# Performance work log

Hardware: AMD Instinct MI355X
Metric: run time of the kernel (lower is better)

## Reference

```python
import jax, jax.numpy as jnp
import numpy as np

B, IN, H = 4096, 512, 1024
ALPHA, RHO = 0.001, 0.05

def setup_inputs() -> dict:
    key = jax.random.key(0)
    ks = jax.random.split(key, 9)
    inp = jax.random.normal(ks[0], (B, IN), dtype=jnp.float32)
    time = jax.random.uniform(ks[1], (B, 1), dtype=jnp.float32) * 100.0
    hx = jax.random.normal(ks[2], (B, H), dtype=jnp.float32)
    cx = jax.random.normal(ks[3], (B, H), dtype=jnp.float32)
    # params (match torch init scales loosely)
    Wxh_w = jax.random.normal(ks[4], (4 * H, IN), dtype=jnp.float32) / np.sqrt(IN)
    Wxh_b = jnp.zeros((4 * H,), dtype=jnp.float32)
    Whh_w = jax.random.normal(ks[5], (4 * H, H), dtype=jnp.float32) / np.sqrt(H)
    tau = jax.random.normal(ks[6], (H,), dtype=jnp.float32) * 0.5 + 5.0
    s = jax.random.uniform(ks[7], (H,), dtype=jnp.float32) * tau
    alpha = jnp.array([ALPHA], dtype=jnp.float32)
    rho = jnp.array([RHO], dtype=jnp.float32)
    return {"input": inp, "time": time, "hx": hx, "cx": cx,
            "Wxh_w": Wxh_w, "Wxh_b": Wxh_b, "Whh_w": Whh_w,
            "tau": tau, "s": s, "alpha": alpha, "rho": rho}

def _time_gate(time, s, tau, alpha, rho):
    # phi: [B, H] (time [B,1] broadcast against s/tau [H])
    phi = jnp.fmod(time - s, tau) / tau
    k = jnp.where(phi < rho / 2.0, 2.0 * phi / rho,
        jnp.where(phi < rho, 2.0 - 2.0 * phi / rho, alpha * phi))
    # computed under torch.no_grad() in the original
    return jax.lax.stop_gradient(k)

def reference(input, time, hx, cx, Wxh_w, Wxh_b, Whh_w, tau, s, alpha, rho):
    gates = input @ Wxh_w.T + Wxh_b + hx @ Whh_w.T  # [B, 4H]
    i, f, g, o = jnp.split(gates, 4, axis=1)
    k = _time_gate(time, s, tau, alpha, rho)
    ft = jax.nn.sigmoid(f + 1.0 - k)
    it = jax.nn.sigmoid(i) * k
    gt = jnp.tanh(g) * k
    ot = jax.nn.sigmoid(o) * k
    cy = ft * cx + it * gt
    hy = ot * jnp.tanh(cy)
    return (hy, cy)
```

## Files before the change

### kernel.cpp

```cpp
#include <hip/hip_runtime.h>

#define AS1 __attribute__((address_space(1)))
#define AS3 __attribute__((address_space(3)))

typedef _Float16 half_t;
typedef __attribute__((ext_vector_type(8))) _Float16 f16x8;
typedef __attribute__((ext_vector_type(4))) float f32x4;

static constexpr int Bsz = 4096;
static constexpr int INs = 512;
static constexpr int Hs  = 1024;
static constexpr int BM  = 128;
static constexpr int BH  = 32;
static constexpr int BK  = 64;

static constexpr size_t XN  = (size_t)Bsz * INs;
static constexpr size_t HXN = (size_t)Bsz * Hs;
static constexpr size_t WXN = (size_t)4 * Hs * INs;
static constexpr size_t WHN = (size_t)4 * Hs * Hs;
static constexpr size_t OFF_X  = 0;
static constexpr size_t OFF_HX = XN;
static constexpr size_t OFF_WX = XN + HXN;
static constexpr size_t OFF_WH = XN + HXN + WXN;
static constexpr size_t TOT    = XN + HXN + WXN + WHN;

__device__ __forceinline__ float sigm(float x) {
  return 1.0f / (1.0f + __expf(-x));
}
__device__ __forceinline__ float tanh_fast(float x) {
  const float e = __expf(2.0f * x);
  return 1.0f - 2.0f / (e + 1.0f);
}

__global__ __launch_bounds__(256)
void cvt_kernel(const float* __restrict__ x, const float* __restrict__ hx,
                const float* __restrict__ wx, const float* __restrict__ wh,
                half_t* __restrict__ ws) {
  const size_t cid = (size_t)blockIdx.x * 256 + threadIdx.x;
  const size_t e = cid * 8;
  const float* src; size_t off;
  if (e < OFF_HX)      { src = x;  off = e - OFF_X; }
  else if (e < OFF_WX) { src = hx; off = e - OFF_HX; }
  else if (e < OFF_WH) { src = wx; off = e - OFF_WX; }
  else                 { src = wh; off = e - OFF_WH; }
  const f32x4 a = *(const f32x4*)(src + off);
  const f32x4 b = *(const f32x4*)(src + off + 4);
  f16x8 o;
  o[0]=(half_t)a[0]; o[1]=(half_t)a[1]; o[2]=(half_t)a[2]; o[3]=(half_t)a[3];
  o[4]=(half_t)b[0]; o[5]=(half_t)b[1]; o[6]=(half_t)b[2]; o[7]=(half_t)b[3];
  *(f16x8*)(ws + e) = o;
}


#define KSTEP(Abase, vA, Wbase, vB, Ka_, t_) do { \
  _Pragma("unroll") \
  for (int i_ = 0; i_ < 4; ++i_) { \
    const int e_ = i_ * 32 + ldr; \
    const half_t* ga_ = (Abase) + (vA) + (i_ * 32 * (Ka_) + (t_) * BK); \
    __builtin_amdgcn_global_load_lds((AS1 void*)ga_, \
        (AS3 void*)(As + (e_ * 8 + ldc) * 8), 16, 0, 0); \
    const half_t* gw_ = (Wbase) + (vB)[i_] + ((t_) * BK); \
    __builtin_amdgcn_global_load_lds((AS1 void*)gw_, \
        (AS3 void*)(Bs + (e_ * 8 + ldc) * 8), 16, 0, 0); \
  } \
  __syncthreads(); \
  _Pragma("unroll") \
  for (int kk_ = 0; kk_ < 2; ++kk_) { \
    const int c8x_ = kk_ * 4 + grp; \
    f16x8 af_[4], bf_[4]; \
    _Pragma("unroll") \
    for (int mt_ = 0; mt_ < 4; ++mt_) { \
      const int e_ = wr * 64 + mt_ * 16 + l15; \
      af_[mt_] = *(const f16x8*)(As + (e_ * 8 + (c8x_ ^ (l15 & 7))) * 8); \
    } \
    _Pragma("unroll") \
    for (int nt_ = 0; nt_ < 4; ++nt_) { \
      const int e_ = wc * 64 + nt_ * 16 + l15; \
      bf_[nt_] = *(const f16x8*)(Bs + (e_ * 8 + (c8x_ ^ (l15 & 7))) * 8); \
    } \
    _Pragma("unroll") \
    for (int mt_ = 0; mt_ < 4; ++mt_) \
      _Pragma("unroll") \
      for (int nt_ = 0; nt_ < 4; ++nt_) \
        acc[mt_][nt_] = __builtin_amdgcn_mfma_f32_16x16x32_f16( \
            af_[mt_], bf_[nt_], acc[mt_][nt_], 0, 0, 0); \
  } \
  __syncthreads(); \
} while (0)

__global__ __launch_bounds__(256, 4)
void plstm_gemm(const half_t* __restrict__ xin,
                const half_t* __restrict__ hxp,
                const float* __restrict__ cxp,
                const half_t* __restrict__ wxh,
                const float* __restrict__ biasp,
                const half_t* __restrict__ whh,
                const float* __restrict__ timep,
                const float* __restrict__ taup,
                const float* __restrict__ sp,
                const float* __restrict__ alphap,
                const float* __restrict__ rhop,
                float* __restrict__ outp)
{
  __shared__ half_t As[BM * BK];
  __shared__ half_t Bs[BM * BK];

  const int tid  = threadIdx.x;
  const int w    = tid >> 6;
  const int lane = tid & 63;
  const int l15  = lane & 15;
  const int grp  = lane >> 4;
  const int wr   = w >> 1;
  const int wc   = w & 1;

  const int m0 = blockIdx.x * BM;
  const int h0 = blockIdx.y * BH;

  f32x4 acc[4][4] = {};

  const int ldr = tid >> 3;
  const int ldc = tid & 7;
  const int gc8 = ldc ^ (ldr & 7);

  {
    const half_t* Ab = xin + (size_t)m0 * INs;
    const int vA = ldr * INs + gc8 * 8;
    int vB[4];
    #pragma unroll
    for (int i = 0; i < 4; ++i) {
      const int gi = (2 * i + (ldr >> 4)) & 3;
      vB[i] = (gi * Hs + h0 + (i >> 1) * 16 + (ldr & 15)) * INs + gc8 * 8;
    }
    #pragma unroll
    for (int t = 0; t < INs / BK; ++t)
      KSTEP(Ab, vA, wxh, vB, INs, t);
  }
  {
    const half_t* Ab = hxp + (size_t)m0 * Hs;
    const int vA = ldr * Hs + gc8 * 8;
    int vB[4];
    #pragma unroll
    for (int i = 0; i < 4; ++i) {
      const int gi = (2 * i + (ldr >> 4)) & 3;
      vB[i] = (gi * Hs + h0 + (i >> 1) * 16 + (ldr & 15)) * Hs + gc8 * 8;
    }
    #pragma unroll
    for (int t = 0; t < Hs / BK; ++t)
      KSTEP(Ab, vA, whh, vB, Hs, t);
  }

  const int h = h0 + wc * 16 + l15;
  const float bi  = biasp[h];
  const float bfv = biasp[Hs + h];
  const float bg  = biasp[2 * Hs + h];
  const float bo  = biasp[3 * Hs + h];
  const float sv = sp[h], tauv = taup[h];
  const float alphav = alphap[0], rhov = rhop[0], rh = 0.5f * rhov;
  const float rtau   = 1.0f / tauv;
  const float tworho = 2.0f / rhov;

  #pragma unroll
  for (int mt = 0; mt < 4; ++mt) {
    const f32x4 t4 = *(const f32x4*)(timep + m0 + wr * 64 + mt * 16 + grp * 4);
    #pragma unroll
    for (int r = 0; r < 4; ++r) {
      const int brow = m0 + wr * 64 + mt * 16 + grp * 4 + r;
      const float q   = (t4[r] - sv) * rtau;
      const float phi = q - truncf(q);
      const float kv  = phi < rh   ? phi * tworho
                      : (phi < rhov ? 2.0f - phi * tworho
                                    : alphav * phi);

      const float iv = acc[mt][0][r] + bi;
      const float fv = acc[mt][1][r] + bfv;
      const float gv = acc[mt][2][r] + bg;
      const float ov = acc[mt][3][r] + bo;
      const float cxv = cxp[(size_t)brow * Hs + h];
      const float ft = sigm(fv + 1.0f - kv);
      const float it2 = sigm(iv) * kv;
      const float gt = tanh_fast(gv) * kv;
      const float ot = sigm(ov) * kv;
      const float cy = ft * cxv + it2 * gt;
      const float hy = ot * tanh_fast(cy);

      outp[(size_t)brow * Hs + h] = hy;
      outp[(size_t)Bsz * Hs + (size_t)brow * Hs + h] = cy;
    }
  }
}

__global__ __launch_bounds__(256, 3)
void plstm_gemm_f32(const float* __restrict__ xin, const float* __restrict__ timep,
                    const float* __restrict__ hxp, const float* __restrict__ cxp,
                    const float* __restrict__ wxh, const float* __restrict__ biasp,
                    const float* __restrict__ whh, const float* __restrict__ taup,
                    const float* __restrict__ sp, const float* __restrict__ alphap,
                    const float* __restrict__ rhop, float* __restrict__ outp)
{
  __shared__ half_t As[BM * BK];
  __shared__ half_t Bs[BM * BK];

  const int tid  = threadIdx.x;
  const int w    = tid >> 6;
  const int lane = tid & 63;
  const int l15  = lane & 15;
  const int grp  = lane >> 4;
  const int wr   = w >> 1;
  const int wc   = w & 1;

  const int m0 = blockIdx.x * BM;
  const int h0 = blockIdx.y * BH;

  f32x4 acc[4][4] = {};
  const int ldr = tid >> 3;
  const int ldc = tid & 7;
  const int NIT = INs / BK + Hs / BK;

  for (int it = 0; it < NIT; ++it) {
    const bool p1 = it >= INs / BK;
    const float* Ap = p1 ? hxp : xin;
    const float* Wp = p1 ? whh : wxh;
    const int Ka = p1 ? Hs : INs;
    const int k0 = (p1 ? (it - INs / BK) : it) * BK;
    #pragma unroll
    for (int i = 0; i < 4; ++i) {
      const int e    = i * 32 + ldr;
      const int gc8  = ldc ^ (e & 7);
      const int wrow = ((e >> 4) & 3) * Hs + h0 + ((e >> 6) << 4) + (e & 15);
      const float* ga = Ap + (size_t)(m0 + e) * Ka + (k0 + gc8 * 8);
      const f32x4 a0v = *(const f32x4*)ga, a1v = *(const f32x4*)(ga + 4);
      f16x8 pa;
      pa[0]=(half_t)a0v[0]; pa[1]=(half_t)a0v[1]; pa[2]=(half_t)a0v[2]; pa[3]=(half_t)a0v[3];
      pa[4]=(half_t)a1v[0]; pa[5]=(half_t)a1v[1]; pa[6]=(half_t)a1v[2]; pa[7]=(half_t)a1v[3];
      *(f16x8*)(As + (e * 8 + ldc) * 8) = pa;
      const float* gw = Wp + (size_t)wrow * Ka + (k0 + gc8 * 8);
      const f32x4 b0v = *(const f32x4*)gw, b1v = *(const f32x4*)(gw + 4);
      f16x8 pb;
      pb[0]=(half_t)b0v[0]; pb[1]=(half_t)b0v[1]; pb[2]=(half_t)b0v[2]; pb[3]=(half_t)b0v[3];
      pb[4]=(half_t)b1v[0]; pb[5]=(half_t)b1v[1]; pb[6]=(half_t)b1v[2]; pb[7]=(half_t)b1v[3];
      *(f16x8*)(Bs + (e * 8 + ldc) * 8) = pb;
    }
    __syncthreads();
    #pragma unroll
    for (int kk = 0; kk < 2; ++kk) {
      const int c8x = kk * 4 + grp;
      f16x8 af[4], bfr[4];
      #pragma unroll
      for (int mt = 0; mt < 4; ++mt) {
        const int e = wr * 64 + mt * 16 + l15;
        af[mt] = *(const f16x8*)(As + (e * 8 + (c8x ^ (l15 & 7))) * 8);
      }
      #pragma unroll
      for (int nt = 0; nt < 4; ++nt) {
        const int e = wc * 64 + nt * 16 + l15;
        bfr[nt] = *(const f16x8*)(Bs + (e * 8 + (c8x ^ (l15 & 7))) * 8);
      }
      #pragma unroll
      for (int mt = 0; mt < 4; ++mt)
        #pragma unroll
        for (int nt = 0; nt < 4; ++nt)
          acc[mt][nt] = __builtin_amdgcn_mfma_f32_16x16x32_f16(
              af[mt], bfr[nt], acc[mt][nt], 0, 0, 0);
    }
    __syncthreads();
  }

  const int h = h0 + wc * 16 + l15;
  const float bi  = biasp[h];
  const float bfv = biasp[Hs + h];
  const float bg  = biasp[2 * Hs + h];
  const float bo  = biasp[3 * Hs + h];
  const float sv = sp[h], tauv = taup[h];
  const float alphav = alphap[0], rhov = rhop[0], rh = 0.5f * rhov;
  const float rtau   = 1.0f / tauv;
  const float tworho = 2.0f / rhov;

  #pragma unroll
  for (int mt = 0; mt < 4; ++mt) {
    const f32x4 t4 = *(const f32x4*)(timep + m0 + wr * 64 + mt * 16 + grp * 4);
    #pragma unroll
    for (int r = 0; r < 4; ++r) {
      const int brow = m0 + wr * 64 + mt * 16 + grp * 4 + r;
      const float q   = (t4[r] - sv) * rtau;
      const float phi = q - truncf(q);
      const float kv  = phi < rh   ? phi * tworho
                      : (phi < rhov ? 2.0f - phi * tworho
                                    : alphav * phi);
      const float iv = acc[mt][0][r] + bi;
      const float fv = acc[mt][1][r] + bfv;
      const float gv = acc[mt][2][r] + bg;
      const float ov = acc[mt][3][r] + bo;
      const float cxv = cxp[(size_t)brow * Hs + h];
      const float ft = sigm(fv + 1.0f - kv);
      const float it2 = sigm(iv) * kv;
      const float gt = tanh_fast(gv) * kv;
      const float ot = sigm(ov) * kv;
      const float cy = ft * cxv + it2 * gt;
      const float hy = ot * tanh_fast(cy);
      outp[(size_t)brow * Hs + h] = hy;
      outp[(size_t)Bsz * Hs + (size_t)brow * Hs + h] = cy;
    }
  }
}

extern "C" void kernel_launch(void* const* d_in, const int* in_sizes, int n_in,
                              void* d_out, int out_size, void* d_ws, size_t ws_size,
                              hipStream_t stream) {
  (void)in_sizes; (void)n_in; (void)out_size;
  const float* xin   = (const float*)d_in[0];
  const float* timep = (const float*)d_in[1];
  const float* hxp   = (const float*)d_in[2];
  const float* cxp   = (const float*)d_in[3];
  const float* wxh   = (const float*)d_in[4];
  const float* biasp = (const float*)d_in[5];
  const float* whh   = (const float*)d_in[6];
  const float* taup  = (const float*)d_in[7];
  const float* sp    = (const float*)d_in[8];
  const float* alphap= (const float*)d_in[9];
  const float* rhop  = (const float*)d_in[10];
  float* outp = (float*)d_out;

  dim3 grid(Bsz / BM, Hs / BH);
  if (ws_size >= TOT * sizeof(half_t)) {
    half_t* ws = (half_t*)d_ws;
    cvt_kernel<<<(int)(TOT / 8 / 256), 256, 0, stream>>>(xin, hxp, wxh, whh, ws);
    plstm_gemm<<<grid, 256, 0, stream>>>(
        ws + OFF_X, ws + OFF_HX, cxp, ws + OFF_WX, biasp, ws + OFF_WH,
        timep, taup, sp, alphap, rhop, outp);
  } else {
    plstm_gemm_f32<<<grid, 256, 0, stream>>>(
        xin, timep, hxp, cxp, wxh, biasp, whh,
        taup, sp, alphap, rhop, outp);
  }
}
```

Before: 180.8 us.

## Double-buffer weight tiles in LDS and load activations directly to registers

The fp16 GEMM kernel stops staging the activation tile through LDS. Each wave now loads its A fragments straight from global memory into registers. Only the weight tile goes through LDS, now in two buffers, so the next k-step's weights are prefetched with global_load_lds while the current step's MFMAs run, leaving one barrier per step instead of two. Occupancy hint drops from 4 to 3 blocks per SM because the extra register fragments and the doubled B buffer raise register and LDS use; direct global A loads may also be less coalesced than the old LDS staging.

```diff
diff --git a/kernel.cpp b/kernel.cpp
--- a/kernel.cpp
+++ b/kernel.cpp
@@ -52,43 +52,40 @@
 }
 
 
-#define KSTEP(Abase, vA, Wbase, vB, Ka_, t_) do { \
+#define GSTEP(bufR, bufW, Ab, vA0, KaA, Wsrc, vBv, STAGE_EN) do { \
+  f16x8 af_[4][2]; \
   _Pragma("unroll") \
-  for (int i_ = 0; i_ < 4; ++i_) { \
-    const int e_ = i_ * 32 + ldr; \
-    const half_t* ga_ = (Abase) + (vA) + (i_ * 32 * (Ka_) + (t_) * BK); \
-    __builtin_amdgcn_global_load_lds((AS1 void*)ga_, \
-        (AS3 void*)(As + (e_ * 8 + ldc) * 8), 16, 0, 0); \
-    const half_t* gw_ = (Wbase) + (vB)[i_] + ((t_) * BK); \
-    __builtin_amdgcn_global_load_lds((AS1 void*)gw_, \
-        (AS3 void*)(Bs + (e_ * 8 + ldc) * 8), 16, 0, 0); \
-  } \
-  __syncthreads(); \
+  for (int mt_ = 0; mt_ < 4; ++mt_) \
+    _Pragma("unroll") \
+    for (int kk_ = 0; kk_ < 2; ++kk_) \
+      af_[mt_][kk_] = *(const f16x8*)((Ab) + (size_t)(mt_ * 16 * (KaA)) + (vA0) + kk_ * 32); \
+  if (STAGE_EN) { \
+    _Pragma("unroll") \
+    for (int i_ = 0; i_ < 4; ++i_) { \
+      const int e_ = i_ * 32 + ldr; \
+      __builtin_amdgcn_global_load_lds((AS1 void*)((Wsrc) + (vBv)[i_]), \
+          (AS3 void*)((bufW) + (e_ * 8 + ldc) * 8), 16, 0, 0); \
+    } } \
   _Pragma("unroll") \
   for (int kk_ = 0; kk_ < 2; ++kk_) { \
     const int c8x_ = kk_ * 4 + grp; \
-    f16x8 af_[4], bf_[4]; \
-    _Pragma("unroll") \
-    for (int mt_ = 0; mt_ < 4; ++mt_) { \
-      const int e_ = wr * 64 + mt_ * 16 + l15; \
-      af_[mt_] = *(const f16x8*)(As + (e_ * 8 + (c8x_ ^ (l15 & 7))) * 8); \
-    } \
+    f16x8 bf_[4]; \
     _Pragma("unroll") \
     for (int nt_ = 0; nt_ < 4; ++nt_) { \
       const int e_ = wc * 64 + nt_ * 16 + l15; \
-      bf_[nt_] = *(const f16x8*)(Bs + (e_ * 8 + (c8x_ ^ (l15 & 7))) * 8); \
+      bf_[nt_] = *(const f16x8*)((bufR) + (e_ * 8 + (c8x_ ^ (l15 & 7))) * 8); \
     } \
     _Pragma("unroll") \
     for (int mt_ = 0; mt_ < 4; ++mt_) \
       _Pragma("unroll") \
       for (int nt_ = 0; nt_ < 4; ++nt_) \
         acc[mt_][nt_] = __builtin_amdgcn_mfma_f32_16x16x32_f16( \
-            af_[mt_], bf_[nt_], acc[mt_][nt_], 0, 0, 0); \
+            af_[mt_][kk_], bf_[nt_], acc[mt_][nt_], 0, 0, 0); \
   } \
   __syncthreads(); \
 } while (0)
 
-__global__ __launch_bounds__(256, 4)
+__global__ __launch_bounds__(256, 3)
 void plstm_gemm(const half_t* __restrict__ xin,
                 const half_t* __restrict__ hxp,
                 const float* __restrict__ cxp,
@@ -102,8 +99,7 @@
                 const float* __restrict__ rhop,
                 float* __restrict__ outp)
 {
-  __shared__ half_t As[BM * BK];
-  __shared__ half_t Bs[BM * BK];
+  __shared__ half_t Bs[2][BM * BK];
 
   const int tid  = threadIdx.x;
   const int w    = tid >> 6;
@@ -122,31 +118,48 @@
   const int ldc = tid & 7;
   const int gc8 = ldc ^ (ldr & 7);
 
+  const int vA0X = (wr * 64 + l15) * INs + grp * 8;
+  const int vA0H = (wr * 64 + l15) * Hs  + grp * 8;
+  int vBX[4], vBH[4];
+  #pragma unroll
+  for (int i = 0; i < 4; ++i) {
+    const int e    = i * 32 + ldr;
+    const int wrow = ((e >> 4) & 3) * Hs + h0 + ((e >> 6) << 4) + (e & 15);
+    vBX[i] = wrow * INs + gc8 * 8;
+    vBH[i] = wrow * Hs  + gc8 * 8;
+  }
+
+  const half_t* xb = xin + (size_t)m0 * INs;
+  const half_t* hb = hxp + (size_t)m0 * Hs;
+
+  #pragma unroll
+  for (int i = 0; i < 4; ++i) {
+    const int e = i * 32 + ldr;
+    __builtin_amdgcn_global_load_lds((AS1 void*)(wxh + vBX[i]),
+        (AS3 void*)(Bs[0] + (e * 8 + ldc) * 8), 16, 0, 0);
+  }
+  __syncthreads();
+
+  #pragma unroll
+  for (int t = 0; t < 8; ++t) {
+    GSTEP(Bs[t & 1], Bs[(t + 1) & 1],
+          xb + t * 64, vA0X, INs,
+          (t == 7 ? whh : wxh + (t + 1) * 64),
+          (t == 7 ? vBH : vBX), true);
+  }
+
   {
-    const half_t* Ab = xin + (size_t)m0 * INs;
-    const int vA = ldr * INs + gc8 * 8;
-    int vB[4];
-    #pragma unroll
-    for (int i = 0; i < 4; ++i) {
-      const int gi = (2 * i + (ldr >> 4)) & 3;
-      vB[i] = (gi * Hs + h0 + (i >> 1) * 16 + (ldr & 15)) * INs + gc8 * 8;
-    }
-    #pragma unroll
-    for (int t = 0; t < INs / BK; ++t)
-      KSTEP(Ab, vA, wxh, vB, INs, t);
-  }
-  {
-    const half_t* Ab = hxp + (size_t)m0 * Hs;
-    const int vA = ldr * Hs + gc8 * 8;
-    int vB[4];
-    #pragma unroll
-    for (int i = 0; i < 4; ++i) {
-      const int gi = (2 * i + (ldr >> 4)) & 3;
-      vB[i] = (gi * Hs + h0 + (i >> 1) * 16 + (ldr & 15)) * Hs + gc8 * 8;
-    }
-    #pragma unroll
-    for (int t = 0; t < Hs / BK; ++t)
-      KSTEP(Ab, vA, whh, vB, Hs, t);
+    const half_t* ha  = hb;
+    const half_t* wsc = whh + 64;
+    #pragma unroll 1
+    for (int i = 0; i < 7; ++i) {
+      GSTEP(Bs[0], Bs[1], ha,      vA0H, Hs, wsc,      vBH, true);
+      GSTEP(Bs[1], Bs[0], ha + 64, vA0H, Hs, wsc + 64, vBH, true);
+      ha  += 128;
+      wsc += 128;
+    }
+    GSTEP(Bs[0], Bs[1], ha,      vA0H, Hs, wsc, vBH, true);
+    GSTEP(Bs[1], Bs[0], ha + 64, vA0H, Hs, whh, vBH, false);
   }
 
   const int h = h0 + wc * 16 + l15;
@@ -198,7 +211,7 @@
                     const float* __restrict__ rhop, float* __restrict__ outp)
 {
   __shared__ half_t As[BM * BK];
-  __shared__ half_t Bs[BM * BK];
+  __shared__ half_t Bsf[BM * BK];
 
   const int tid  = threadIdx.x;
   const int w    = tid >> 6;
@@ -238,7 +251,7 @@
       f16x8 pb;
       pb[0]=(half_t)b0v[0]; pb[1]=(half_t)b0v[1]; pb[2]=(half_t)b0v[2]; pb[3]=(half_t)b0v[3];
       pb[4]=(half_t)b1v[0]; pb[5]=(half_t)b1v[1]; pb[6]=(half_t)b1v[2]; pb[7]=(half_t)b1v[3];
-      *(f16x8*)(Bs + (e * 8 + ldc) * 8) = pb;
+      *(f16x8*)(Bsf + (e * 8 + ldc) * 8) = pb;
     }
     __syncthreads();
     #pragma unroll
@@ -253,7 +266,7 @@
       #pragma unroll
       for (int nt = 0; nt < 4; ++nt) {
         const int e = wc * 64 + nt * 16 + l15;
-        bfr[nt] = *(const f16x8*)(Bs + (e * 8 + (c8x ^ (l15 & 7))) * 8);
+        bfr[nt] = *(const f16x8*)(Bsf + (e * 8 + (c8x ^ (l15 & 7))) * 8);
       }
       #pragma unroll
       for (int mt = 0; mt < 4; ++mt)
```

New measurement: 259.3 us. 1.43x slower.
